# Performance work log

Hardware: AMD Instinct MI355X
Metric: run time of the kernel (lower is better)

## Reference

```python
import jax, jax.numpy as jnp
import numpy as np

B, S, D, H, DH, DK = 2, 2048, 1024, 16, 64, 64


def setup_inputs() -> dict:
    key = jax.random.key(0)
    ks = jax.random.split(key, 11)
    scale_in = 1.0 / np.sqrt(D)
    return {
        "Q": jax.random.normal(ks[0], (B, S, D), jnp.float32),
        "K": jax.random.normal(ks[1], (B, S, D), jnp.float32),
        "V": jax.random.normal(ks[2], (B, S, D), jnp.float32),
        "Wq": jax.random.normal(ks[3], (H, D, DH), jnp.float32) * scale_in,
        "bq": jax.random.normal(ks[4], (H, DH), jnp.float32) * 0.02,
        "Wk": jax.random.normal(ks[5], (H, D, DH), jnp.float32) * scale_in,
        "bk": jax.random.normal(ks[6], (H, DH), jnp.float32) * 0.02,
        "Wv": jax.random.normal(ks[7], (H, D, DH), jnp.float32) * scale_in,
        "bv": jax.random.normal(ks[8], (H, DH), jnp.float32) * 0.02,
        "Wf": jax.random.normal(ks[9], (D, D), jnp.float32) * scale_in,
        "bf": jax.random.normal(ks[10], (D,), jnp.float32) * 0.02,
    }


def reference(Q, K, V, Wq, bq, Wk, bk, Wv, bv, Wf, bf):
    # Per-head projections, vectorized over the head axis h. [B,H,S,DH]
    Qh = jnp.einsum("bsd,hde->bhse", Q, Wq) + bq[None, :, None, :]
    Kh = jnp.einsum("bsd,hde->bhse", K, Wk) + bk[None, :, None, :]
    Vh = jnp.einsum("bsd,hde->bhse", V, Wv) + bv[None, :, None, :]
    inv_sqrt_dk = jnp.asarray(1.0 / np.sqrt(DK), Qh.dtype)
    # Full attention matrix [B,H,S,S] (faithful to the naive original).
    scores = jnp.einsum("bhse,bhte->bhst", Qh, Kh) * inv_sqrt_dk
    attn = jax.nn.softmax(scores, axis=-1)  # F.softmax default -> last dim
    out = jnp.einsum("bhst,bhte->bhse", attn, Vh)  # [B,H,S,DH]
    # Concat heads on the feature axis: [B,S,H*DH] == [B,S,D]
    out = out.transpose(0, 2, 1, 3).reshape(Q.shape[0], Q.shape[1], -1)
    return out @ Wf + bf
```

## Files before the change

kernel.cpp:

```cpp
#include <hip/hip_runtime.h>

#define DEV __device__ __forceinline__

typedef unsigned short u16;
typedef unsigned int   u32;
typedef __attribute__((ext_vector_type(4)))  float f32x4;
typedef __attribute__((ext_vector_type(8)))  short s16x8;
typedef __attribute__((ext_vector_type(2)))  u32   u32x2;

static constexpr size_t OFF_QBF  = 0;
static constexpr size_t OFF_KBF  = 8388608;
static constexpr size_t OFF_VBF  = 16777216;
static constexpr size_t OFF_WCAT = 25165824;
static constexpr size_t OFF_WFT  = 31457280;
static constexpr size_t OFF_BIAS = 33554432;
static constexpr size_t OFF_QKVH = 33566720;
static constexpr size_t OFF_VT   = 58732544;
static constexpr size_t OFF_OBUF = 67121152;

DEV u16 f2bf(float f) {
  union { float f; u32 u; } a; a.f = f;
  u32 r = a.u + 0x7FFFu + ((a.u >> 16) & 1u);
  return (u16)(r >> 16);
}
DEV u32 f2bf2(float lo, float hi_) {
  return (u32)f2bf(lo) | ((u32)f2bf(hi_) << 16);
}

#if __has_builtin(__builtin_amdgcn_exp2f)
DEV float fast_exp2(float x) { return __builtin_amdgcn_exp2f(x); }
#else
DEV float fast_exp2(float x) { return exp2f(x); }
#endif

DEV f32x4 mfma16(s16x8 a, s16x8 b, f32x4 c) {
  return __builtin_amdgcn_mfma_f32_16x16x32_bf16(a, b, c, 0, 0, 0);
}

DEV void gload_lds16(const void* g, void* l) {
  __builtin_amdgcn_global_load_lds(
      (__attribute__((address_space(1))) void*)g,
      (__attribute__((address_space(3))) void*)l, 16, 0, 0);
}

__global__ __launch_bounds__(256) void prep_all_k(const float* __restrict__ Q,
                                                  const float* __restrict__ K,
                                                  const float* __restrict__ V,
                                                  const float* __restrict__ Wq,
                                                  const float* __restrict__ Wk,
                                                  const float* __restrict__ Wv,
                                                  const float* __restrict__ Wf,
                                                  const float* __restrict__ bq,
                                                  const float* __restrict__ bk,
                                                  const float* __restrict__ bv,
                                                  u16* __restrict__ QKVbf,
                                                  u16* __restrict__ Wcat,
                                                  u16* __restrict__ WfT,
                                                  float* __restrict__ biascat) {
  const int bid = blockIdx.x;
  __shared__ u16 t[64][72];
  if (bid < 12288) {
    size_t idx = (size_t)bid * 256 + threadIdx.x;
    size_t tt  = idx >> 20;
    size_t r   = idx & 1048575;
    const float* src = (tt == 0) ? Q : (tt == 1) ? K : V;
    f32x4 v = *(const f32x4*)(src + r * 4);
    u32x2 o;
    o[0] = f2bf2(v[0], v[1]);
    o[1] = f2bf2(v[2], v[3]);
    *(u32x2*)(QKVbf + idx * 4) = o;
  } else if (bid < 13056) {
    const int q = bid - 12288;
    const int dt = q & 15, h = (q >> 4) & 15, z = q >> 8;
    const float* W = (z == 0) ? Wq : (z == 1) ? Wk : Wv;
#pragma unroll
    for (int p = 0; p < 16; ++p) {
      int idx = threadIdx.x + p * 256;
      int r = idx >> 6, e = idx & 63;
      t[r][e] = f2bf(W[((size_t)h * 1024 + dt * 64 + r) * 64 + e]);
    }
    __syncthreads();
#pragma unroll
    for (int p = 0; p < 16; ++p) {
      int idx = threadIdx.x + p * 256;
      int e = idx >> 6, r = idx & 63;
      Wcat[((size_t)z * 1024 + h * 64 + e) * 1024 + dt * 64 + r] = t[r][e];
    }
  } else if (bid < 13312) {
    const int q = bid - 13056;
    const int dt = q & 15, ft = q >> 4;
#pragma unroll
    for (int p = 0; p < 16; ++p) {
      int idx = threadIdx.x + p * 256;
      int r = idx >> 6, f = idx & 63;
      t[r][f] = f2bf(Wf[(size_t)(dt * 64 + r) * 1024 + ft * 64 + f]);
    }
    __syncthreads();
#pragma unroll
    for (int p = 0; p < 16; ++p) {
      int idx = threadIdx.x + p * 256;
      int f = idx >> 6, r = idx & 63;
      WfT[(size_t)(ft * 64 + f) * 1024 + dt * 64 + r] = t[r][f];
    }
  } else {
    int i = (bid - 13312) * 256 + threadIdx.x;
    if (i < 1024) biascat[i] = bq[i];
    else if (i < 2048) biascat[i] = bk[i - 1024];
    else if (i < 3072) biascat[i] = bv[i - 2048];
  }
}

template <int MODE>
DEV void gemm128(const u16* __restrict__ A, int lda,
                 const u16* __restrict__ B, int ldb,
                 const float* __restrict__ bias,
                 void* __restrict__ Cp, size_t ldc, int K) {
  __shared__ u16 Ash[128 * 32];
  __shared__ u16 Bsh[128 * 32];
  const int tid = threadIdx.x;
  const int lane = tid & 63;
  const int w = tid >> 6;
  const int wr = w >> 1, wc = w & 1;
  const int lr = lane >> 2;
  const int lc = (lane & 3) << 3;
  const int l15 = lane & 15, lg = lane >> 4;

  f32x4 acc[4][4];
#pragma unroll
  for (int i = 0; i < 4; ++i)
#pragma unroll
    for (int j = 0; j < 4; ++j) acc[i][j] = f32x4{0.f, 0.f, 0.f, 0.f};

  for (int kt = 0; kt < K; kt += 32) {
    if (kt) __syncthreads();
#pragma unroll
    for (int j = 0; j < 2; ++j) {
      const u16* ga = A + (size_t)(w * 32 + j * 16 + lr) * lda + kt + lc;
      gload_lds16(ga, (char*)Ash + (w * 2 + j) * 1024);
      const u16* gb = B + (size_t)(w * 32 + j * 16 + lr) * ldb + kt + lc;
      gload_lds16(gb, (char*)Bsh + (w * 2 + j) * 1024);
    }
    __syncthreads();
    s16x8 af[4], bv_[4];
#pragma unroll
    for (int i = 0; i < 4; ++i) {
      af[i]  = *(const s16x8*)&Ash[(wr * 64 + i * 16 + l15) * 32 + lg * 8];
      bv_[i] = *(const s16x8*)&Bsh[(wc * 64 + i * 16 + l15) * 32 + lg * 8];
    }
#pragma unroll
    for (int mf = 0; mf < 4; ++mf)
#pragma unroll
      for (int nf = 0; nf < 4; ++nf)
        acc[mf][nf] = mfma16(af[mf], bv_[nf], acc[mf][nf]);
  }
#pragma unroll
  for (int nf = 0; nf < 4; ++nf) {
    const int nn = wc * 64 + nf * 16 + l15;
    const float bvv = bias[nn];
#pragma unroll
    for (int mf = 0; mf < 4; ++mf) {
      if (MODE == 2) {
        const int mm0 = wr * 64 + mf * 16 + lg * 4;
        u32x2 d;
        d[0] = f2bf2(acc[mf][nf][0] + bvv, acc[mf][nf][1] + bvv);
        d[1] = f2bf2(acc[mf][nf][2] + bvv, acc[mf][nf][3] + bvv);
        *(u32x2*)((u16*)Cp + (size_t)nn * ldc + mm0) = d;
      } else {
#pragma unroll
        for (int j = 0; j < 4; ++j) {
          const int mm = wr * 64 + mf * 16 + lg * 4 + j;
          float v = acc[mf][nf][j] + bvv;
          if (MODE == 1) ((u16*)Cp)[(size_t)mm * ldc + nn] = f2bf(v);
          else           ((float*)Cp)[(size_t)mm * ldc + nn] = v;
        }
      }
    }
  }
}

__global__ __launch_bounds__(256) void proj_gemm_k(const u16* __restrict__ Qb,
                                                   const u16* __restrict__ Kb,
                                                   const u16* __restrict__ Vb,
                                                   const u16* __restrict__ Wcat,
                                                   const float* __restrict__ biascat,
                                                   u16* __restrict__ QKVh,
                                                   u16* __restrict__ Vt) {
  const int z = blockIdx.z;
  const u16* A = (z == 0) ? Qb : (z == 1) ? Kb : Vb;
  const int m0 = blockIdx.y * 128;
  const int nl = blockIdx.x * 128;
  if (z == 2) {
    gemm128<2>(A + (size_t)m0 * 1024, 1024,
               Wcat + (size_t)(2 * 1024 + nl) * 1024, 1024,
               biascat + 2 * 1024 + nl,
               Vt + (size_t)nl * 4096 + m0, 4096, 1024);
  } else {
    gemm128<1>(A + (size_t)m0 * 1024, 1024,
               Wcat + (size_t)(z * 1024 + nl) * 1024, 1024,
               biascat + z * 1024 + nl,
               QKVh + (size_t)m0 * 3072 + z * 1024 + nl, 3072, 1024);
  }
}

__global__ __launch_bounds__(256) void final_gemm_k(const u16* __restrict__ Obuf,
                                                    const u16* __restrict__ WfT,
                                                    const float* __restrict__ bf,
                                                    float* __restrict__ out) {
  const int m0 = blockIdx.y * 128;
  const int n0 = blockIdx.x * 128;
  gemm128<0>(Obuf + (size_t)m0 * 1024, 1024,
             WfT + (size_t)n0 * 1024, 1024,
             bf + n0,
             out + (size_t)m0 * 1024 + n0, 1024, 1024);
}

__global__ __launch_bounds__(512) void attn9_k(const u16* __restrict__ QKVh,
                                               const u16* __restrict__ Vt,
                                               u16* __restrict__ Obuf) {
  const int id = blockIdx.x;
  const int virt = (id & 7) * 64 + (id >> 3);
  const int qb = virt & 15;
  const int hb = virt >> 4;
  const int h = hb & 15, b = hb >> 4;

  const int tid = threadIdx.x, lane = tid & 63, w = tid >> 6;
  const int l15 = lane & 15, lg = lane >> 4;

  __shared__ u16 Ksh[2][64 * 64];
  __shared__ u16 Vsh[2][64 * 64];
  __shared__ u16 Psh[8][16 * 64];

  const size_t rowQ = (size_t)(b * 2048 + qb * 128);
  const u16* Qbase = QKVh + rowQ * 3072 + h * 64;
  const u16* Kbase = QKVh + (size_t)(b * 2048) * 3072 + 1024 + h * 64;
  const u16* Vbase = Vt + (size_t)(h * 64) * 4096 + b * 2048;

  s16x8 aq[2];
#pragma unroll
  for (int kf = 0; kf < 2; ++kf)
    aq[kf] = *(const s16x8*)(Qbase + (size_t)(w * 16 + l15) * 3072 + kf * 32 + lg * 8);

  f32x4 accO[4];
  f32x4 lacc = f32x4{0.f, 0.f, 0.f, 0.f};
#pragma unroll
  for (int nf = 0; nf < 4; ++nf) accO[nf] = f32x4{0.f, 0.f, 0.f, 0.f};

  const float CSC = 0.18033688011112042f;
  const float M2 = 12.0f;
  const s16x8 ONESV = {0x3F80, 0x3F80, 0x3F80, 0x3F80,
                       0x3F80, 0x3F80, 0x3F80, 0x3F80};

  const int sr = tid >> 3, ch = tid & 7;
  const int sswz = (sr & 7) << 4;
  const u16* Kg = Kbase + (size_t)sr * 3072 + ch * 8;
  const u16* Vg = Vbase + (size_t)sr * 4096 + ch * 8;

  s16x8 kreg0 = *(const s16x8*)Kg;
  s16x8 kreg1 = *(const s16x8*)(Kg + (size_t)64 * 3072);
  s16x8 vreg0 = *(const s16x8*)Vg;
  s16x8 vreg1 = *(const s16x8*)(Vg + 64);
  Kg += (size_t)128 * 3072;
  Vg += 128;

  for (int kt2 = 0; kt2 < 16; ++kt2) {
    if (kt2) __syncthreads();
    *(s16x8*)((char*)&Ksh[0][0] + sr * 128 + ((ch * 16) ^ sswz)) = kreg0;
    *(s16x8*)((char*)&Ksh[1][0] + sr * 128 + ((ch * 16) ^ sswz)) = kreg1;
    *(s16x8*)((char*)&Vsh[0][0] + sr * 128 + ((ch * 16) ^ sswz)) = vreg0;
    *(s16x8*)((char*)&Vsh[1][0] + sr * 128 + ((ch * 16) ^ sswz)) = vreg1;
    __syncthreads();

    if (kt2 < 15) {
      kreg0 = *(const s16x8*)Kg;
      kreg1 = *(const s16x8*)(Kg + (size_t)64 * 3072);
      vreg0 = *(const s16x8*)Vg;
      vreg1 = *(const s16x8*)(Vg + 64);
      Kg += (size_t)128 * 3072;
      Vg += 128;
    }

#pragma unroll
    for (int u = 0; u < 2; ++u) {
      const char* kbuf = (const char*)&Ksh[u][0];
      const char* vbuf = (const char*)&Vsh[u][0];

      f32x4 sc[4];
#pragma unroll
      for (int nf = 0; nf < 4; ++nf) sc[nf] = f32x4{0.f, 0.f, 0.f, 0.f};
#pragma unroll
      for (int kf = 0; kf < 2; ++kf) {
        s16x8 kb[4];
#pragma unroll
        for (int nf = 0; nf < 4; ++nf) {
          int row = nf * 16 + l15;
          kb[nf] = *(const s16x8*)(kbuf + row * 128 + ((kf * 64 + lg * 16) ^ ((row & 7) << 4)));
        }
#pragma unroll
        for (int nf = 0; nf < 4; ++nf)
          sc[nf] = mfma16(aq[kf], kb[nf], sc[nf]);
      }

#pragma unroll
      for (int nf = 0; nf < 4; ++nf)
#pragma unroll
        for (int j = 0; j < 4; ++j)
          sc[nf][j] = fast_exp2(fmaf(sc[nf][j], CSC, -M2));

      char* pbase = (char*)&Psh[w][0];
#pragma unroll
      for (int nf = 0; nf < 4; ++nf)
#pragma unroll
        for (int j = 0; j < 4; ++j) {
          int srow = lg * 4 + j;
          int tcol = nf * 16 + l15;
          *(u16*)(pbase + srow * 128 + ((tcol * 2) ^ ((srow & 7) << 4))) =
              f2bf(sc[nf][j]);
        }
      asm volatile("s_waitcnt lgkmcnt(0)" ::: "memory");
      __builtin_amdgcn_sched_barrier(0);

#pragma unroll
      for (int kf = 0; kf < 2; ++kf) {
        s16x8 pa, vb[4];
        pa = *(const s16x8*)(pbase + l15 * 128 + ((kf * 64 + lg * 16) ^ ((l15 & 7) << 4)));
#pragma unroll
        for (int nf = 0; nf < 4; ++nf) {
          int row = nf * 16 + l15;
          vb[nf] = *(const s16x8*)(vbuf + row * 128 + ((kf * 64 + lg * 16) ^ ((row & 7) << 4)));
        }
#pragma unroll
        for (int nf = 0; nf < 4; ++nf)
          accO[nf] = mfma16(pa, vb[nf], accO[nf]);
        lacc = mfma16(pa, ONESV, lacc);
      }
    }
  }

  u16* Ob = Obuf + rowQ * 1024 + h * 64;
  float inv[4];
#pragma unroll
  for (int j = 0; j < 4; ++j) inv[j] = 1.f / lacc[j];
#pragma unroll
  for (int nf = 0; nf < 4; ++nf)
#pragma unroll
    for (int j = 0; j < 4; ++j)
      Ob[(size_t)(w * 16 + lg * 4 + j) * 1024 + nf * 16 + l15] =
          f2bf(accO[nf][j] * inv[j]);
}

extern "C" void kernel_launch(void* const* d_in, const int* in_sizes, int n_in,
                              void* d_out, int out_size, void* d_ws, size_t ws_size,
                              hipStream_t stream) {
  const float* Q  = (const float*)d_in[0];
  const float* K  = (const float*)d_in[1];
  const float* V  = (const float*)d_in[2];
  const float* Wq = (const float*)d_in[3];
  const float* bq = (const float*)d_in[4];
  const float* Wk = (const float*)d_in[5];
  const float* bk = (const float*)d_in[6];
  const float* Wv = (const float*)d_in[7];
  const float* bv = (const float*)d_in[8];
  const float* Wf = (const float*)d_in[9];
  const float* bf = (const float*)d_in[10];
  float* out = (float*)d_out;
  char* ws = (char*)d_ws;

  u16*   QKVbf  = (u16*)(ws + OFF_QBF);
  u16*   Qbf    = (u16*)(ws + OFF_QBF);
  u16*   Kbf    = (u16*)(ws + OFF_KBF);
  u16*   Vbf    = (u16*)(ws + OFF_VBF);
  u16*   Wcat   = (u16*)(ws + OFF_WCAT);
  u16*   WfT    = (u16*)(ws + OFF_WFT);
  float* biascat= (float*)(ws + OFF_BIAS);
  u16*   QKVh   = (u16*)(ws + OFF_QKVH);
  u16*   Vt     = (u16*)(ws + OFF_VT);
  u16*   Obuf   = (u16*)(ws + OFF_OBUF);

  dim3 blk(256);
  prep_all_k<<<13324, blk, 0, stream>>>(Q, K, V, Wq, Wk, Wv, Wf, bq, bk, bv,
                                        QKVbf, Wcat, WfT, biascat);
  proj_gemm_k<<<dim3(8, 32, 3), blk, 0, stream>>>(Qbf, Kbf, Vbf, Wcat, biascat,
                                                  QKVh, Vt);
  attn9_k<<<dim3(512), dim3(512), 0, stream>>>(QKVh, Vt, Obuf);
  final_gemm_k<<<dim3(8, 32), blk, 0, stream>>>(Obuf, WfT, bf, out);
}
```

Before: 136.7 us.

## Fuse fp32-to-bf16 input conversion into projection GEMM and remap blocks per XCD

Drops the separate pass that converted Q/K/V from fp32 to bf16 in the prep kernel. The projection GEMM now loads fp32 A tiles into registers, prefetches the next k-tile after the barrier, and converts to bf16 while writing to LDS. This removes a 48MB read plus 24MB write-and-reread round trip. Both GEMM grids are flattened to 1D and remapped so that consecutive blocks landing on the same XCD share row panels, which should improve L2 reuse. In exchange the A loads in the projection GEMM now go through registers rather than direct-to-LDS loads, which adds register pressure and fp32 read traffic repeated across the 8 column blocks.

```diff
diff --git a/kernel.cpp b/kernel.cpp
--- a/kernel.cpp
+++ b/kernel.cpp
@@ -8,9 +8,6 @@
 typedef __attribute__((ext_vector_type(8)))  short s16x8;
 typedef __attribute__((ext_vector_type(2)))  u32   u32x2;
 
-static constexpr size_t OFF_QBF  = 0;
-static constexpr size_t OFF_KBF  = 8388608;
-static constexpr size_t OFF_VBF  = 16777216;
 static constexpr size_t OFF_WCAT = 25165824;
 static constexpr size_t OFF_WFT  = 31457280;
 static constexpr size_t OFF_BIAS = 33554432;
@@ -43,34 +40,20 @@
       (__attribute__((address_space(3))) void*)l, 16, 0, 0);
 }
 
-__global__ __launch_bounds__(256) void prep_all_k(const float* __restrict__ Q,
-                                                  const float* __restrict__ K,
-                                                  const float* __restrict__ V,
-                                                  const float* __restrict__ Wq,
+__global__ __launch_bounds__(256) void prep_all_k(const float* __restrict__ Wq,
                                                   const float* __restrict__ Wk,
                                                   const float* __restrict__ Wv,
                                                   const float* __restrict__ Wf,
                                                   const float* __restrict__ bq,
                                                   const float* __restrict__ bk,
                                                   const float* __restrict__ bv,
-                                                  u16* __restrict__ QKVbf,
                                                   u16* __restrict__ Wcat,
                                                   u16* __restrict__ WfT,
                                                   float* __restrict__ biascat) {
   const int bid = blockIdx.x;
   __shared__ u16 t[64][72];
-  if (bid < 12288) {
-    size_t idx = (size_t)bid * 256 + threadIdx.x;
-    size_t tt  = idx >> 20;
-    size_t r   = idx & 1048575;
-    const float* src = (tt == 0) ? Q : (tt == 1) ? K : V;
-    f32x4 v = *(const f32x4*)(src + r * 4);
-    u32x2 o;
-    o[0] = f2bf2(v[0], v[1]);
-    o[1] = f2bf2(v[2], v[3]);
-    *(u32x2*)(QKVbf + idx * 4) = o;
-  } else if (bid < 13056) {
-    const int q = bid - 12288;
+  if (bid < 768) {
+    const int q = bid;
     const int dt = q & 15, h = (q >> 4) & 15, z = q >> 8;
     const float* W = (z == 0) ? Wq : (z == 1) ? Wk : Wv;
 #pragma unroll
@@ -86,8 +69,8 @@
       int e = idx >> 6, r = idx & 63;
       Wcat[((size_t)z * 1024 + h * 64 + e) * 1024 + dt * 64 + r] = t[r][e];
     }
-  } else if (bid < 13312) {
-    const int q = bid - 13056;
+  } else if (bid < 1024) {
+    const int q = bid - 768;
     const int dt = q & 15, ft = q >> 4;
 #pragma unroll
     for (int p = 0; p < 16; ++p) {
@@ -103,15 +86,15 @@
       WfT[(size_t)(ft * 64 + f) * 1024 + dt * 64 + r] = t[r][f];
     }
   } else {
-    int i = (bid - 13312) * 256 + threadIdx.x;
+    int i = (bid - 1024) * 256 + threadIdx.x;
     if (i < 1024) biascat[i] = bq[i];
     else if (i < 2048) biascat[i] = bk[i - 1024];
     else if (i < 3072) biascat[i] = bv[i - 2048];
   }
 }
 
-template <int MODE>
-DEV void gemm128(const u16* __restrict__ A, int lda,
+template <int MODE, int AF32>
+DEV void gemm128(const void* __restrict__ Ap, int lda,
                  const u16* __restrict__ B, int ldb,
                  const float* __restrict__ bias,
                  void* __restrict__ Cp, size_t ldc, int K) {
@@ -125,22 +108,51 @@
   const int lc = (lane & 3) << 3;
   const int l15 = lane & 15, lg = lane >> 4;
 
+  const u16*   A16 = (const u16*)Ap;
+  const float* A32 = (const float*)Ap;
+  const int ar = lane >> 3, ac = lane & 7;
+
   f32x4 acc[4][4];
 #pragma unroll
   for (int i = 0; i < 4; ++i)
 #pragma unroll
     for (int j = 0; j < 4; ++j) acc[i][j] = f32x4{0.f, 0.f, 0.f, 0.f};
+
+  f32x4 areg[4];
+  if (AF32) {
+#pragma unroll
+    for (int p = 0; p < 4; ++p)
+      areg[p] = *(const f32x4*)(A32 + (size_t)(w * 32 + p * 8 + ar) * lda + ac * 4);
+  }
 
   for (int kt = 0; kt < K; kt += 32) {
     if (kt) __syncthreads();
+    if (AF32) {
+#pragma unroll
+      for (int p = 0; p < 4; ++p) {
+        u32x2 o;
+        o[0] = f2bf2(areg[p][0], areg[p][1]);
+        o[1] = f2bf2(areg[p][2], areg[p][3]);
+        *(u32x2*)((char*)Ash + (w * 32 + p * 8 + ar) * 64 + ac * 8) = o;
+      }
+    } else {
+#pragma unroll
+      for (int j = 0; j < 2; ++j) {
+        const u16* ga = A16 + (size_t)(w * 32 + j * 16 + lr) * lda + kt + lc;
+        gload_lds16(ga, (char*)Ash + (w * 2 + j) * 1024);
+      }
+    }
 #pragma unroll
     for (int j = 0; j < 2; ++j) {
-      const u16* ga = A + (size_t)(w * 32 + j * 16 + lr) * lda + kt + lc;
-      gload_lds16(ga, (char*)Ash + (w * 2 + j) * 1024);
       const u16* gb = B + (size_t)(w * 32 + j * 16 + lr) * ldb + kt + lc;
       gload_lds16(gb, (char*)Bsh + (w * 2 + j) * 1024);
     }
     __syncthreads();
+    if (AF32 && kt + 32 < K) {
+#pragma unroll
+      for (int p = 0; p < 4; ++p)
+        areg[p] = *(const f32x4*)(A32 + (size_t)(w * 32 + p * 8 + ar) * lda + kt + 32 + ac * 4);
+    }
     s16x8 af[4], bv_[4];
 #pragma unroll
     for (int i = 0; i < 4; ++i) {
@@ -178,27 +190,31 @@
   }
 }
 
-__global__ __launch_bounds__(256) void proj_gemm_k(const u16* __restrict__ Qb,
-                                                   const u16* __restrict__ Kb,
-                                                   const u16* __restrict__ Vb,
+__global__ __launch_bounds__(256) void proj_gemm_k(const float* __restrict__ Qf,
+                                                   const float* __restrict__ Kf,
+                                                   const float* __restrict__ Vf,
                                                    const u16* __restrict__ Wcat,
                                                    const float* __restrict__ biascat,
                                                    u16* __restrict__ QKVh,
                                                    u16* __restrict__ Vt) {
-  const int z = blockIdx.z;
-  const u16* A = (z == 0) ? Qb : (z == 1) ? Kb : Vb;
-  const int m0 = blockIdx.y * 128;
-  const int nl = blockIdx.x * 128;
+  const int F = blockIdx.x;
+  const int xcd = F & 7, i = F >> 3;
+  const int panel = xcd * 12 + (i >> 3);
+  const int x = i & 7;
+  const int y = panel & 31, z = panel >> 5;
+  const float* A = (z == 0) ? Qf : (z == 1) ? Kf : Vf;
+  const int m0 = y * 128;
+  const int nl = x * 128;
   if (z == 2) {
-    gemm128<2>(A + (size_t)m0 * 1024, 1024,
-               Wcat + (size_t)(2 * 1024 + nl) * 1024, 1024,
-               biascat + 2 * 1024 + nl,
-               Vt + (size_t)nl * 4096 + m0, 4096, 1024);
+    gemm128<2, 1>(A + (size_t)m0 * 1024, 1024,
+                  Wcat + (size_t)(2 * 1024 + nl) * 1024, 1024,
+                  biascat + 2 * 1024 + nl,
+                  Vt + (size_t)nl * 4096 + m0, 4096, 1024);
   } else {
-    gemm128<1>(A + (size_t)m0 * 1024, 1024,
-               Wcat + (size_t)(z * 1024 + nl) * 1024, 1024,
-               biascat + z * 1024 + nl,
-               QKVh + (size_t)m0 * 3072 + z * 1024 + nl, 3072, 1024);
+    gemm128<1, 1>(A + (size_t)m0 * 1024, 1024,
+                  Wcat + (size_t)(z * 1024 + nl) * 1024, 1024,
+                  biascat + z * 1024 + nl,
+                  QKVh + (size_t)m0 * 3072 + z * 1024 + nl, 3072, 1024);
   }
 }
 
@@ -206,12 +222,16 @@
                                                     const u16* __restrict__ WfT,
                                                     const float* __restrict__ bf,
                                                     float* __restrict__ out) {
-  const int m0 = blockIdx.y * 128;
-  const int n0 = blockIdx.x * 128;
-  gemm128<0>(Obuf + (size_t)m0 * 1024, 1024,
-             WfT + (size_t)n0 * 1024, 1024,
-             bf + n0,
-             out + (size_t)m0 * 1024 + n0, 1024, 1024);
+  const int F = blockIdx.x;
+  const int xcd = F & 7, i = F >> 3;
+  const int panel = xcd * 4 + (i >> 3);
+  const int x = i & 7;
+  const int m0 = panel * 128;
+  const int n0 = x * 128;
+  gemm128<0, 0>(Obuf + (size_t)m0 * 1024, 1024,
+                WfT + (size_t)n0 * 1024, 1024,
+                bf + n0,
+                out + (size_t)m0 * 1024 + n0, 1024, 1024);
 }
 
 __global__ __launch_bounds__(512) void attn9_k(const u16* __restrict__ QKVh,
@@ -365,10 +385,6 @@
   float* out = (float*)d_out;
   char* ws = (char*)d_ws;
 
-  u16*   QKVbf  = (u16*)(ws + OFF_QBF);
-  u16*   Qbf    = (u16*)(ws + OFF_QBF);
-  u16*   Kbf    = (u16*)(ws + OFF_KBF);
-  u16*   Vbf    = (u16*)(ws + OFF_VBF);
   u16*   Wcat   = (u16*)(ws + OFF_WCAT);
   u16*   WfT    = (u16*)(ws + OFF_WFT);
   float* biascat= (float*)(ws + OFF_BIAS);
@@ -377,10 +393,9 @@
   u16*   Obuf   = (u16*)(ws + OFF_OBUF);
 
   dim3 blk(256);
-  prep_all_k<<<13324, blk, 0, stream>>>(Q, K, V, Wq, Wk, Wv, Wf, bq, bk, bv,
-                                        QKVbf, Wcat, WfT, biascat);
-  proj_gemm_k<<<dim3(8, 32, 3), blk, 0, stream>>>(Qbf, Kbf, Vbf, Wcat, biascat,
-                                                  QKVh, Vt);
+  prep_all_k<<<1036, blk, 0, stream>>>(Wq, Wk, Wv, Wf, bq, bk, bv,
+                                       Wcat, WfT, biascat);
+  proj_gemm_k<<<768, blk, 0, stream>>>(Q, K, V, Wcat, biascat, QKVh, Vt);
   attn9_k<<<dim3(512), dim3(512), 0, stream>>>(QKVh, Vt, Obuf);
-  final_gemm_k<<<dim3(8, 32), blk, 0, stream>>>(Obuf, WfT, bf, out);
-}
+  final_gemm_k<<<256, blk, 0, stream>>>(Obuf, WfT, bf, out);
+}
```

After: 128.5 us (median of 2 runs). -5.9%, faster.
